# Optimization experiments

Measured on AMD Instinct MI355X. Metric: run time of the kernel, lower is better.

Reference implementation:

```python
import jax, jax.numpy as jnp
import numpy as np

ATT_HEAD, IN_DIM, OUT_DIM = 8, 768, 96
B, N = 8, 1024
LEAKY_ALPHA = 0.2


def setup_inputs() -> dict:
    key = jax.random.key(0)
    ks = jax.random.split(key, 8)
    feat_in = jax.random.normal(ks[0], (B, N, IN_DIM), dtype=jnp.float32)
    adj = jax.random.randint(ks[1], (B, N, N), 0, 2).astype(jnp.float32)
    # xavier-ish init scales
    W = jax.random.normal(ks[2], (ATT_HEAD, IN_DIM, OUT_DIM), dtype=jnp.float32) * (1.0 / np.sqrt(IN_DIM))
    b = jnp.zeros((OUT_DIM,), dtype=jnp.float32)
    w_src = jax.random.normal(ks[3], (ATT_HEAD, OUT_DIM, 1), dtype=jnp.float32) * (1.0 / np.sqrt(OUT_DIM))
    w_dst = jax.random.normal(ks[4], (ATT_HEAD, OUT_DIM, 1), dtype=jnp.float32) * (1.0 / np.sqrt(OUT_DIM))
    Hw = jax.random.normal(ks[5], (IN_DIM, IN_DIM), dtype=jnp.float32) * (1.0 / np.sqrt(IN_DIM))
    Hb = jnp.zeros((IN_DIM,), dtype=jnp.float32)
    return {"feat_in": feat_in, "adj": adj, "W": W, "b": b,
            "w_src": w_src, "w_dst": w_dst, "Hw": Hw, "Hb": Hb}


def reference(feat_in, adj, W, b, w_src, w_dst, Hw, Hb):
    batch, n, _ = feat_in.shape
    # per-head projection: [B,H,N,O]
    h = jnp.einsum('bni,hio->bhno', feat_in, W)
    t = jnp.tanh(h)
    a_src = jnp.einsum('bhno,hoq->bhnq', t, w_src)[..., 0]  # [B,H,N]
    a_dst = jnp.einsum('bhno,hoq->bhnq', t, w_dst)[..., 0]  # [B,H,N]
    attn = a_src[:, :, :, None] + a_dst[:, :, None, :]       # [B,H,N,N]
    attn = jnp.where(attn >= 0, attn, LEAKY_ALPHA * attn)
    mask = adj[:, None, :, :] == 0                            # 1-adj as bool
    attn = jnp.where(mask, jnp.float32(-999.0), attn)
    attn = jax.nn.softmax(attn, axis=-1)
    feat_out = jnp.einsum('bhnm,bhmo->bhno', attn, h) + b     # [B,H,N,O]
    feat_out = jnp.transpose(feat_out, (0, 2, 1, 3)).reshape(batch, n, -1)
    feat_out = jax.nn.elu(feat_out)
    gate = jax.nn.sigmoid(feat_in @ Hw.T + Hb)
    return gate * feat_out + (1.0 - gate) * feat_in
```

## Files before the change

### kernel.cpp

```cpp
#include <hip/hip_runtime.h>
#include <cstddef>

#define BATCH 8
#define NN 1024
#define IN_DIM 768
#define OUT_DIM 96
#define HEADS 8
#define M_ROWS 8192
#define NCOLS 1536

typedef __attribute__((ext_vector_type(8))) short short8;
typedef __attribute__((ext_vector_type(4))) float f32x4;
typedef __attribute__((ext_vector_type(4))) unsigned short ushort4v;
typedef _Float16 half8 __attribute__((ext_vector_type(8)));

typedef __attribute__((address_space(1))) void gvoid_t;
typedef __attribute__((address_space(3))) void lvoid_t;

__device__ __forceinline__ void gload_lds16(const void* g, void* l) {
    __builtin_amdgcn_global_load_lds((gvoid_t*)(unsigned long long)g,
                                     (lvoid_t*)(unsigned int)(unsigned long long)l,
                                     16, 0, 0);
}

__device__ __forceinline__ unsigned int pkrtz(float a, float b) {
    return __builtin_bit_cast(unsigned int, __builtin_amdgcn_cvt_pkrtz(a, b));
}
__device__ __forceinline__ unsigned short f2h(float x) {
    _Float16 h = (_Float16)x;
    return __builtin_bit_cast(unsigned short, h);
}
__device__ __forceinline__ float h2f(unsigned short u) {
    return (float)__builtin_bit_cast(_Float16, u);
}
__device__ __forceinline__ float tanh_fast(float x) {
    return 1.f - 2.f / (__expf(2.f * x) + 1.f);
}
__device__ __forceinline__ f32x4 mfma16(short8 a, short8 b, f32x4 c) {
    return __builtin_amdgcn_mfma_f32_16x16x32_f16(
        __builtin_bit_cast(half8, a), __builtin_bit_cast(half8, b), c, 0, 0, 0);
}

__global__ __launch_bounds__(256) void prep_kernel(
        const float* __restrict__ feat_in, const float* __restrict__ W,
        const float* __restrict__ Hw, const float* __restrict__ adj,
        unsigned short* __restrict__ Xb, unsigned short* __restrict__ BT,
        unsigned int* __restrict__ abits, float* __restrict__ a_zero) {
    int blk = blockIdx.x;
    int t = threadIdx.x;
    if (blk < 3072) {
        int idx = blk * 256 + t;
        const float4* p = (const float4*)(feat_in + (size_t)idx * 8);
        float4 a = p[0], b = p[1];
        union { unsigned int u4[4]; short8 s8; } pk;
        pk.u4[0] = pkrtz(a.x, a.y);
        pk.u4[1] = pkrtz(a.z, a.w);
        pk.u4[2] = pkrtz(b.x, b.y);
        pk.u4[3] = pkrtz(b.z, b.w);
        *(short8*)(Xb + (size_t)idx * 8) = pk.s8;
    } else if (blk < 5376) {
        int idx = (blk - 3072) * 256 + t;
        int c = idx / IN_DIM, i = idx % IN_DIM;
        int h = c / OUT_DIM, o = c % OUT_DIM;
        BT[(size_t)c * IN_DIM + i] = f2h(W[((size_t)h * IN_DIM + i) * OUT_DIM + o]);
    } else if (blk < 7680) {
        int idx = (blk - 5376) * 256 + t;
        int c = idx / IN_DIM, i = idx % IN_DIM;
        BT[(size_t)(768 + c) * IN_DIM + i] = f2h(Hw[(size_t)c * IN_DIM + i]);
    } else if (blk < 8704) {
        int idx = (blk - 7680) * 256 + t;
        const float4* p = (const float4*)(adj + (size_t)idx * 32);
        unsigned int m = 0;
        #pragma unroll
        for (int q = 0; q < 8; ++q) {
            float4 v = p[q];
            m |= (v.x != 0.f ? 1u : 0u) << (q * 4 + 0);
            m |= (v.y != 0.f ? 1u : 0u) << (q * 4 + 1);
            m |= (v.z != 0.f ? 1u : 0u) << (q * 4 + 2);
            m |= (v.w != 0.f ? 1u : 0u) << (q * 4 + 3);
        }
        abits[idx] = m;
    } else {
        int idx = (blk - 8704) * 256 + t;
        f32x4 z = {0.f, 0.f, 0.f, 0.f};
        *(f32x4*)(a_zero + (size_t)idx * 8) = z;
        *(f32x4*)(a_zero + (size_t)idx * 8 + 4) = z;
    }
}

__global__ __launch_bounds__(256) void gemm1_kernel(
        const unsigned short* __restrict__ Xb, const unsigned short* __restrict__ BT,
        const float* __restrict__ Hb, const float* __restrict__ w_src,
        const float* __restrict__ w_dst,
        unsigned short* __restrict__ h_bt, unsigned short* __restrict__ gate,
        float* __restrict__ a_src, float* __restrict__ a_dst) {
    __shared__ __align__(16) unsigned short As[2][128 * 32];
    __shared__ __align__(16) unsigned short Bs[2][128 * 32];
    __shared__ float hbs[128];
    __shared__ float ws_s[128], wd_s[128];
    int m0 = blockIdx.x * 128;
    int c0 = blockIdx.y * 128;
    int t = threadIdx.x;
    int w = t >> 6, lane = t & 63, l15 = t & 15, quad = lane >> 4;
    if (c0 >= 768) {
        if (t < 128) hbs[t] = Hb[c0 - 768 + t];
    } else {
        if (t < 128) {
            int c = c0 + t;
            int hd = c / OUT_DIM, o = c % OUT_DIM;
            ws_s[t] = w_src[hd * OUT_DIM + o];
            wd_s[t] = w_dst[hd * OUT_DIM + o];
        }
    }
    int uA0 = w * 2, uA1 = w * 2 + 1;
    int rA0 = uA0 * 16 + (lane >> 2), rA1 = uA1 * 16 + (lane >> 2);
    int qb = (lane & 3) ^ ((lane >> 3) & 3);
    int qo = qb * 8;
    const unsigned short* gA0 = Xb + (size_t)(m0 + rA0) * IN_DIM + qo;
    const unsigned short* gA1 = Xb + (size_t)(m0 + rA1) * IN_DIM + qo;
    const unsigned short* gB0 = BT + (size_t)(c0 + rA0) * IN_DIM + qo;
    const unsigned short* gB1 = BT + (size_t)(c0 + rA1) * IN_DIM + qo;
    int swz = (quad ^ ((l15 >> 1) & 3)) * 8;
    int aoff0 = (w * 32 + l15) * 32 + swz;
    int aoff1 = aoff0 + 16 * 32;
    int boff  = l15 * 32 + swz;

    f32x4 acc[2][8] = {};

    auto stage = [&](unsigned short* Ad, unsigned short* Bd, int koff) {
        gload_lds16(gA0 + koff, Ad + uA0 * 512);
        gload_lds16(gA1 + koff, Ad + uA1 * 512);
        gload_lds16(gB0 + koff, Bd + uA0 * 512);
        gload_lds16(gB1 + koff, Bd + uA1 * 512);
    };
    auto compute = [&](const unsigned short* Ab, const unsigned short* Bb) {
        short8 af0 = *(const short8*)(Ab + aoff0);
        short8 af1 = *(const short8*)(Ab + aoff1);
        #pragma unroll
        for (int nt = 0; nt < 8; ++nt) {
            short8 bfr = *(const short8*)(Bb + boff + nt * 512);
            acc[0][nt] = mfma16(af0, bfr, acc[0][nt]);
            acc[1][nt] = mfma16(af1, bfr, acc[1][nt]);
        }
    };

    stage(&As[0][0], &Bs[0][0], 0);
    __syncthreads();
    for (int ts = 0; ts < 24; ts += 2) {
        stage(&As[1][0], &Bs[1][0], (ts + 1) * 32);
        compute(&As[0][0], &Bs[0][0]);
        __syncthreads();
        if (ts + 2 < 24) stage(&As[0][0], &Bs[0][0], (ts + 2) * 32);
        compute(&As[1][0], &Bs[1][0]);
        __syncthreads();
    }

    int b = m0 >> 10;
    if (c0 < 768) {
        int split = (c0 / 96 + 1) * 96 - c0;
        int headlo = c0 / 96;
        #pragma unroll
        for (int mt = 0; mt < 2; ++mt) {
            int rowbase = m0 + w * 32 + mt * 16 + quad * 4;
            int nbase = rowbase & 1023;
            #pragma unroll
            for (int nt = 0; nt < 8; ++nt) {
                int c = c0 + nt * 16 + l15;
                int hh = c / OUT_DIM, o = c % OUT_DIM;
                union { unsigned int u2[2]; ushort4v u4; } pk;
                pk.u2[0] = pkrtz(acc[mt][nt][0], acc[mt][nt][1]);
                pk.u2[1] = pkrtz(acc[mt][nt][2], acc[mt][nt][3]);
                *(ushort4v*)(h_bt + ((size_t)(b * 8 + hh) * OUT_DIM + o) * NN + nbase) = pk.u4;
            }
            #pragma unroll
            for (int reg = 0; reg < 4; ++reg) {
                float psA = 0.f, pdA = 0.f, psB = 0.f, pdB = 0.f;
                #pragma unroll
                for (int nt = 0; nt < 8; ++nt) {
                    int cl = nt * 16 + l15;
                    float th = tanh_fast(acc[mt][nt][reg]);
                    float s = th * ws_s[cl], d = th * wd_s[cl];
                    if (cl < split) { psA += s; pdA += d; }
                    else            { psB += s; pdB += d; }
                }
                #pragma unroll
                for (int mk = 1; mk <= 8; mk <<= 1) {
                    psA += __shfl_xor(psA, mk); pdA += __shfl_xor(pdA, mk);
                    psB += __shfl_xor(psB, mk); pdB += __shfl_xor(pdB, mk);
                }
                if (l15 == 0) {
                    int n2 = nbase + reg;
                    int ilo = (b * 8 + headlo) * 1024 + n2;
                    atomicAdd(&a_src[ilo], psA * 1.44269504f);
                    atomicAdd(&a_dst[ilo], pdA * 1.44269504f);
                    atomicAdd(&a_src[ilo + 1024], psB * 1.44269504f);
                    atomicAdd(&a_dst[ilo + 1024], pdB * 1.44269504f);
                }
            }
        }
    } else {
        #pragma unroll
        for (int mt = 0; mt < 2; ++mt) {
            int rowbase = m0 + w * 32 + mt * 16 + quad * 4;
            #pragma unroll
            for (int nt = 0; nt < 8; ++nt) {
                int cl = nt * 16 + l15;
                int cg = c0 - 768 + cl;
                #pragma unroll
                for (int reg = 0; reg < 4; ++reg) {
                    float z = acc[mt][nt][reg] + hbs[cl];
                    float g = __builtin_amdgcn_rcpf(1.f + __builtin_amdgcn_exp2f(-1.44269504f * z));
                    gate[(size_t)(rowbase + reg) * 768 + cg] = f2h(g);
                }
            }
        }
    }
}

__global__ __launch_bounds__(512) void attn_kernel(
        const unsigned short* __restrict__ h_bt, const unsigned int* __restrict__ abits,
        const float* __restrict__ a_src_g, const float* __restrict__ a_dst_g,
        const unsigned short* __restrict__ gate, const unsigned short* __restrict__ Xb,
        const float* __restrict__ bias, float* __restrict__ out) {
    __shared__ __align__(16) unsigned short hs[2][96 * 64];
    __shared__ __align__(16) float adst[1024];
    __shared__ float bias_s[96];
    int blk = blockIdx.x;
    int bh = (blk & 7) * 8 + ((blk >> 3) & 7);
    int i0 = (blk >> 6) * 128;
    int b = bh >> 3, hh = bh & 7;
    int t = threadIdx.x;
    int w = t >> 6, lane = t & 63, l15 = t & 15, quad = lane >> 4;
    if (t < 256) *(f32x4*)(adst + t * 4) = *(const f32x4*)(a_dst_g + bh * 1024 + t * 4);
    if (t < 96) bias_s[t] = bias[t];
    int irow = i0 + w * 16 + l15;
    float si = a_src_g[bh * 1024 + irow];
    const unsigned short* hhp = h_bt + (size_t)bh * 96 * NN;
    if (w < 6) {
        #pragma unroll
        for (int cc = 0; cc < 2; ++cc) {
            int u0 = (w * 2 + cc) * 64;
            int p = u0 + lane;
            int r = p >> 3, qs = p & 7, qb = qs ^ (r & 7);
            gload_lds16(hhp + (size_t)r * NN + qb * 8, (char*)&hs[0][0] + (size_t)u0 * 16);
        }
    }
    const unsigned int* mrow = abits + ((size_t)b * NN + irow) * 32;
    uint2 mw = *(const uint2*)(mrow);
    f32x4 acc[7] = {};
    short8 ones = {};
    if (l15 == 0) {
        #pragma unroll
        for (int u = 0; u < 8; ++u) ones[u] = (short)0x3C00;
    }
    __syncthreads();
    for (int j0 = 0; j0 < 1024; j0 += 64) {
        int cur = (j0 >> 6) & 1;
        int jn = j0 + 64;
        if (jn < 1024 && w < 6) {
            #pragma unroll
            for (int cc = 0; cc < 2; ++cc) {
                int u0 = (w * 2 + cc) * 64;
                int p = u0 + lane;
                int r = p >> 3, qs = p & 7, qb = qs ^ (r & 7);
                gload_lds16(hhp + (size_t)r * NN + jn + qb * 8, (char*)&hs[cur ^ 1][0] + (size_t)u0 * 16);
            }
        }
        short8 af[2];
        unsigned int mws[2] = {mw.x, mw.y};
        #pragma unroll
        for (int ks = 0; ks < 2; ++ks) {
            unsigned int byte = (mws[ks] >> (quad * 8)) & 0xFFu;
            f32x4 d0 = *(const f32x4*)(&adst[j0 + ks * 32 + quad * 8]);
            f32x4 d1 = *(const f32x4*)(&adst[j0 + ks * 32 + quad * 8 + 4]);
            float dv[8] = {d0[0], d0[1], d0[2], d0[3], d1[0], d1[1], d1[2], d1[3]};
            float ev[8];
            #pragma unroll
            for (int u = 0; u < 8; ++u) {
                float s = si + dv[u];
                float l = fmaxf(s, 0.2f * s);
                float e = __builtin_amdgcn_exp2f(l);
                ev[u] = ((byte >> u) & 1u) ? e : 0.f;
            }
            union { unsigned int u4[4]; short8 s8; } pk;
            pk.u4[0] = pkrtz(ev[0], ev[1]);
            pk.u4[1] = pkrtz(ev[2], ev[3]);
            pk.u4[2] = pkrtz(ev[4], ev[5]);
            pk.u4[3] = pkrtz(ev[6], ev[7]);
            af[ks] = pk.s8;
        }
        if (jn < 1024) mw = *(const uint2*)(mrow + (jn >> 5));
        #pragma unroll
        for (int ks = 0; ks < 2; ++ks) {
            #pragma unroll
            for (int nt = 0; nt < 6; ++nt) {
                int r = nt * 16 + l15;
                int qs = (ks * 4 + quad) ^ (r & 7);
                short8 bfr = *(const short8*)(&hs[cur][(size_t)(r * 8 + qs) * 8]);
                acc[nt] = mfma16(af[ks], bfr, acc[nt]);
            }
            acc[6] = mfma16(af[ks], ones, acc[6]);
        }
        __syncthreads();
    }
    int rowq = i0 + w * 16 + quad * 4;
    #pragma unroll
    for (int reg = 0; reg < 4; ++reg) {
        float ssum = __shfl(acc[6][reg], (lane & 48));
        float inv = (ssum > 0.f) ? __builtin_amdgcn_rcpf(ssum) : 0.f;
        int n = rowq + reg;
        size_t mrow_o = ((size_t)b * NN + n) * 768 + hh * 96;
        #pragma unroll
        for (int nt = 0; nt < 6; ++nt) {
            int cl = nt * 16 + l15;
            float v = acc[nt][reg] * inv + bias_s[cl];
            float e = (v > 0.f) ? v : (__builtin_amdgcn_exp2f(v * 1.44269504f) - 1.f);
            float g = h2f(gate[mrow_o + cl]);
            float x = h2f(Xb[mrow_o + cl]);
            out[mrow_o + cl] = x + g * (e - x);
        }
    }
}

extern "C" void kernel_launch(void* const* d_in, const int* in_sizes, int n_in,
                              void* d_out, int out_size, void* d_ws, size_t ws_size,
                              hipStream_t stream) {
    const float* feat_in = (const float*)d_in[0];
    const float* adj     = (const float*)d_in[1];
    const float* W       = (const float*)d_in[2];
    const float* bbias   = (const float*)d_in[3];
    const float* w_src   = (const float*)d_in[4];
    const float* w_dst   = (const float*)d_in[5];
    const float* Hw      = (const float*)d_in[6];
    const float* Hb      = (const float*)d_in[7];
    float* out = (float*)d_out;
    char* base = (char*)d_ws;

    unsigned short* Xb    = (unsigned short*)(base);
    unsigned short* BcatT = (unsigned short*)(base + 12582912);
    unsigned short* h_bt  = (unsigned short*)(base + 14942208);
    unsigned short* gate  = (unsigned short*)(base + 27525120);
    float* a_src = (float*)(base + 40108032);
    float* a_dst = (float*)(base + 40370176);
    unsigned int* abits = (unsigned int*)(base + 40632320);

    prep_kernel<<<8768, 256, 0, stream>>>(feat_in, W, Hw, adj, Xb, BcatT, abits, a_src);
    gemm1_kernel<<<dim3(M_ROWS / 128, NCOLS / 128), 256, 0, stream>>>(
        Xb, BcatT, Hb, w_src, w_dst, h_bt, gate, a_src, a_dst);
    attn_kernel<<<64 * 8, 512, 0, stream>>>(h_bt, abits, a_src, a_dst, gate, Xb, bbias, out);
}
```

Before: 184.5 us.

## Process two row tiles per attention block and ballot-pack adjacency bits

The attention kernel now handles 256 query rows per block in two 128-row halves. Each staged h tile in LDS is reused for twice as many MFMAs, which halves h loads and block count (512 to 256 blocks). Separately, adjacency bitmask packing in the prep kernel now uses coalesced per-lane loads plus wave ballots instead of each thread reading 32 contiguous floats. The risks are higher register pressure from doubled accumulators and fewer blocks than CUs on a 256-CU part.

```diff
diff --git a/kernel.cpp b/kernel.cpp
--- a/kernel.cpp
+++ b/kernel.cpp
@@ -68,18 +68,25 @@
         int c = idx / IN_DIM, i = idx % IN_DIM;
         BT[(size_t)(768 + c) * IN_DIM + i] = f2h(Hw[(size_t)c * IN_DIM + i]);
     } else if (blk < 8704) {
-        int idx = (blk - 7680) * 256 + t;
-        const float4* p = (const float4*)(adj + (size_t)idx * 32);
-        unsigned int m = 0;
-        #pragma unroll
-        for (int q = 0; q < 8; ++q) {
-            float4 v = p[q];
-            m |= (v.x != 0.f ? 1u : 0u) << (q * 4 + 0);
-            m |= (v.y != 0.f ? 1u : 0u) << (q * 4 + 1);
-            m |= (v.z != 0.f ? 1u : 0u) << (q * 4 + 2);
-            m |= (v.w != 0.f ? 1u : 0u) << (q * 4 + 3);
-        }
-        abits[idx] = m;
+        int blkr = blk - 7680;
+        int wv = t >> 6, ln = t & 63;
+        const float* arow = adj + ((size_t)blkr * 8 + wv * 2) * 1024;
+        #pragma unroll
+        for (int rr = 0; rr < 2; ++rr) {
+            unsigned long long mym = 0;
+            #pragma unroll
+            for (int it = 0; it < 16; ++it) {
+                float v = arow[rr * 1024 + it * 64 + ln];
+                unsigned long long m = __ballot(v != 0.f);
+                if (ln == it) mym = m;
+            }
+            if (ln < 16) {
+                uint2 st;
+                st.x = (unsigned int)mym;
+                st.y = (unsigned int)(mym >> 32);
+                *(uint2*)(abits + ((size_t)blkr * 8 + wv * 2 + rr) * 32 + ln * 2) = st;
+            }
+        }
     } else {
         int idx = (blk - 8704) * 256 + t;
         f32x4 z = {0.f, 0.f, 0.f, 0.f};
@@ -227,32 +234,52 @@
     __shared__ float bias_s[96];
     int blk = blockIdx.x;
     int bh = (blk & 7) * 8 + ((blk >> 3) & 7);
-    int i0 = (blk >> 6) * 128;
+    int i0 = (blk >> 6) * 256;
     int b = bh >> 3, hh = bh & 7;
     int t = threadIdx.x;
     int w = t >> 6, lane = t & 63, l15 = t & 15, quad = lane >> 4;
     if (t < 256) *(f32x4*)(adst + t * 4) = *(const f32x4*)(a_dst_g + bh * 1024 + t * 4);
     if (t < 96) bias_s[t] = bias[t];
-    int irow = i0 + w * 16 + l15;
-    float si = a_src_g[bh * 1024 + irow];
+    int irowA = i0 + w * 16 + l15;
+    int irowB = irowA + 128;
+    float siA = a_src_g[bh * 1024 + irowA];
+    float siB = a_src_g[bh * 1024 + irowB];
     const unsigned short* hhp = h_bt + (size_t)bh * 96 * NN;
     if (w < 6) {
         #pragma unroll
         for (int cc = 0; cc < 2; ++cc) {
             int u0 = (w * 2 + cc) * 64;
             int p = u0 + lane;
-            int r = p >> 3, qs = p & 7, qb = qs ^ (r & 7);
-            gload_lds16(hhp + (size_t)r * NN + qb * 8, (char*)&hs[0][0] + (size_t)u0 * 16);
-        }
-    }
-    const unsigned int* mrow = abits + ((size_t)b * NN + irow) * 32;
-    uint2 mw = *(const uint2*)(mrow);
-    f32x4 acc[7] = {};
+            int r = p >> 3, qs = p & 7, qqb = qs ^ (r & 7);
+            gload_lds16(hhp + (size_t)r * NN + qqb * 8, (char*)&hs[0][0] + (size_t)u0 * 16);
+        }
+    }
+    const unsigned int* mrowA = abits + ((size_t)b * NN + irowA) * 32;
+    const unsigned int* mrowB = abits + ((size_t)b * NN + irowB) * 32;
+    uint2 mwA = *(const uint2*)(mrowA);
+    uint2 mwB = *(const uint2*)(mrowB);
+    f32x4 accA[7] = {}, accB[7] = {};
     short8 ones = {};
     if (l15 == 0) {
         #pragma unroll
         for (int u = 0; u < 8; ++u) ones[u] = (short)0x3C00;
     }
+    auto build_af = [&](unsigned int byte, float si, const float* dvp) -> short8 {
+        float ev[8];
+        #pragma unroll
+        for (int u = 0; u < 8; ++u) {
+            float s = si + dvp[u];
+            float l = fmaxf(s, 0.2f * s);
+            float e = __builtin_amdgcn_exp2f(l);
+            ev[u] = ((byte >> u) & 1u) ? e : 0.f;
+        }
+        union { unsigned int u4[4]; short8 s8; } pk;
+        pk.u4[0] = pkrtz(ev[0], ev[1]);
+        pk.u4[1] = pkrtz(ev[2], ev[3]);
+        pk.u4[2] = pkrtz(ev[4], ev[5]);
+        pk.u4[3] = pkrtz(ev[6], ev[7]);
+        return pk.s8;
+    };
     __syncthreads();
     for (int j0 = 0; j0 < 1024; j0 += 64) {
         int cur = (j0 >> 6) & 1;
@@ -262,34 +289,27 @@
             for (int cc = 0; cc < 2; ++cc) {
                 int u0 = (w * 2 + cc) * 64;
                 int p = u0 + lane;
-                int r = p >> 3, qs = p & 7, qb = qs ^ (r & 7);
-                gload_lds16(hhp + (size_t)r * NN + jn + qb * 8, (char*)&hs[cur ^ 1][0] + (size_t)u0 * 16);
-            }
-        }
-        short8 af[2];
-        unsigned int mws[2] = {mw.x, mw.y};
+                int r = p >> 3, qs = p & 7, qqb = qs ^ (r & 7);
+                gload_lds16(hhp + (size_t)r * NN + jn + qqb * 8, (char*)&hs[cur ^ 1][0] + (size_t)u0 * 16);
+            }
+        }
+        short8 afA[2], afB[2];
+        unsigned int mwsA[2] = {mwA.x, mwA.y};
+        unsigned int mwsB[2] = {mwB.x, mwB.y};
         #pragma unroll
         for (int ks = 0; ks < 2; ++ks) {
-            unsigned int byte = (mws[ks] >> (quad * 8)) & 0xFFu;
             f32x4 d0 = *(const f32x4*)(&adst[j0 + ks * 32 + quad * 8]);
             f32x4 d1 = *(const f32x4*)(&adst[j0 + ks * 32 + quad * 8 + 4]);
             float dv[8] = {d0[0], d0[1], d0[2], d0[3], d1[0], d1[1], d1[2], d1[3]};
-            float ev[8];
-            #pragma unroll
-            for (int u = 0; u < 8; ++u) {
-                float s = si + dv[u];
-                float l = fmaxf(s, 0.2f * s);
-                float e = __builtin_amdgcn_exp2f(l);
-                ev[u] = ((byte >> u) & 1u) ? e : 0.f;
-            }
-            union { unsigned int u4[4]; short8 s8; } pk;
-            pk.u4[0] = pkrtz(ev[0], ev[1]);
-            pk.u4[1] = pkrtz(ev[2], ev[3]);
-            pk.u4[2] = pkrtz(ev[4], ev[5]);
-            pk.u4[3] = pkrtz(ev[6], ev[7]);
-            af[ks] = pk.s8;
-        }
-        if (jn < 1024) mw = *(const uint2*)(mrow + (jn >> 5));
+            unsigned int byA = (mwsA[ks] >> (quad * 8)) & 0xFFu;
+            unsigned int byB = (mwsB[ks] >> (quad * 8)) & 0xFFu;
+            afA[ks] = build_af(byA, siA, dv);
+            afB[ks] = build_af(byB, siB, dv);
+        }
+        if (jn < 1024) {
+            mwA = *(const uint2*)(mrowA + (jn >> 5));
+            mwB = *(const uint2*)(mrowB + (jn >> 5));
+        }
         #pragma unroll
         for (int ks = 0; ks < 2; ++ks) {
             #pragma unroll
@@ -297,29 +317,35 @@
                 int r = nt * 16 + l15;
                 int qs = (ks * 4 + quad) ^ (r & 7);
                 short8 bfr = *(const short8*)(&hs[cur][(size_t)(r * 8 + qs) * 8]);
-                acc[nt] = mfma16(af[ks], bfr, acc[nt]);
-            }
-            acc[6] = mfma16(af[ks], ones, acc[6]);
+                accA[nt] = mfma16(afA[ks], bfr, accA[nt]);
+                accB[nt] = mfma16(afB[ks], bfr, accB[nt]);
+            }
+            accA[6] = mfma16(afA[ks], ones, accA[6]);
+            accB[6] = mfma16(afB[ks], ones, accB[6]);
         }
         __syncthreads();
     }
-    int rowq = i0 + w * 16 + quad * 4;
-    #pragma unroll
-    for (int reg = 0; reg < 4; ++reg) {
-        float ssum = __shfl(acc[6][reg], (lane & 48));
-        float inv = (ssum > 0.f) ? __builtin_amdgcn_rcpf(ssum) : 0.f;
-        int n = rowq + reg;
-        size_t mrow_o = ((size_t)b * NN + n) * 768 + hh * 96;
-        #pragma unroll
-        for (int nt = 0; nt < 6; ++nt) {
-            int cl = nt * 16 + l15;
-            float v = acc[nt][reg] * inv + bias_s[cl];
-            float e = (v > 0.f) ? v : (__builtin_amdgcn_exp2f(v * 1.44269504f) - 1.f);
-            float g = h2f(gate[mrow_o + cl]);
-            float x = h2f(Xb[mrow_o + cl]);
-            out[mrow_o + cl] = x + g * (e - x);
-        }
-    }
+    auto epilog = [&](const f32x4 (&ac)[7], int rowoff) {
+        int rowq = i0 + rowoff + w * 16 + quad * 4;
+        #pragma unroll
+        for (int reg = 0; reg < 4; ++reg) {
+            float ssum = __shfl(ac[6][reg], (lane & 48));
+            float inv = (ssum > 0.f) ? __builtin_amdgcn_rcpf(ssum) : 0.f;
+            int n = rowq + reg;
+            size_t mrow_o = ((size_t)b * NN + n) * 768 + hh * 96;
+            #pragma unroll
+            for (int nt = 0; nt < 6; ++nt) {
+                int cl = nt * 16 + l15;
+                float v = ac[nt][reg] * inv + bias_s[cl];
+                float e = (v > 0.f) ? v : (__builtin_amdgcn_exp2f(v * 1.44269504f) - 1.f);
+                float g = h2f(gate[mrow_o + cl]);
+                float x = h2f(Xb[mrow_o + cl]);
+                out[mrow_o + cl] = x + g * (e - x);
+            }
+        }
+    };
+    epilog(accA, 0);
+    epilog(accB, 128);
 }
 
 extern "C" void kernel_launch(void* const* d_in, const int* in_sizes, int n_in,
@@ -347,5 +373,5 @@
     prep_kernel<<<8768, 256, 0, stream>>>(feat_in, W, Hw, adj, Xb, BcatT, abits, a_src);
     gemm1_kernel<<<dim3(M_ROWS / 128, NCOLS / 128), 256, 0, stream>>>(
         Xb, BcatT, Hb, w_src, w_dst, h_bt, gate, a_src, a_dst);
-    attn_kernel<<<64 * 8, 512, 0, stream>>>(h_bt, abits, a_src, a_dst, gate, Xb, bbias, out);
-}
+    attn_kernel<<<256, 512, 0, stream>>>(h_bt, abits, a_src, a_dst, gate, Xb, bbias, out);
+}
```

Result: no change. 181.5 us (-1.6%).
